# Optimization experiments

Measured on AMD Instinct MI355X. Metric: run time of the kernel, lower is better.

Reference implementation:

```python
import jax, jax.numpy as jnp
import numpy as np

N, L, D = 8192, 50, 64          # batch nodes, history length, embed_dim
NUM_ITEMS, NUM_ATTRS, NUM_FAM = 50000, 100000, 100000


def setup_inputs() -> dict:
    key = jax.random.key(0)
    ks = jax.random.split(key, 12)
    scale = 0.05
    return {
        "nodes": jax.random.randint(ks[0], (N,), 0, NUM_ITEMS),
        "history_va": jax.random.randint(ks[1], (N, L), 0, NUM_ATTRS),
        "history_af": jax.random.randint(ks[2], (N, L), 0, NUM_FAM),
        "v2e_w": jax.random.normal(ks[3], (NUM_ITEMS, D), jnp.float32) * scale,
        "a2e_w": jax.random.normal(ks[4], (NUM_ATTRS, D), jnp.float32) * scale,
        "f2e_w": jax.random.normal(ks[5], (NUM_FAM, D), jnp.float32) * scale,
        "W1": jax.random.normal(ks[6], (3 * D, D), jnp.float32) * scale,
        "b1": jnp.zeros((D,), jnp.float32),
        "W2": jax.random.normal(ks[7], (D, D), jnp.float32) * scale,
        "b2": jnp.zeros((D,), jnp.float32),
        "w3": jax.random.normal(ks[8], (D, 1), jnp.float32) * scale,
        "b3": jnp.zeros((1,), jnp.float32),
    }


def reference(nodes, history_va, history_af, v2e_w, a2e_w, f2e_w,
              W1, b1, W2, b2, w3, b3):
    # Batched form of the per-node loop (va=True branch).
    e_va = a2e_w[history_va]                       # [N, L, D] gathered attr embeds
    e_af = f2e_w[history_af]                       # [N, L, D] gathered famous embeds
    va_rep = v2e_w[nodes]                          # [N, D]    target item embed
    rep = jnp.broadcast_to(va_rep[:, None, :], e_va.shape)
    x = jnp.concatenate([e_va, rep, e_af], axis=-1)  # [N, L, 3D]
    h = jax.nn.relu(x @ W1 + b1)                   # [N, L, D]
    h = jax.nn.relu(h @ W2 + b2)                   # [N, L, D]
    scores = (h @ w3 + b3)[..., 0]                 # [N, L]
    att = jax.nn.softmax(scores, axis=1)           # softmax over history dim
    # e_va.T @ att per node  ==  weighted sum over history
    return jnp.einsum("nld,nl->nd", e_va, att)     # [N, D]
```

## Files before the change

### kernel.cpp

```cpp
#include <hip/hip_runtime.h>
#include <hip/hip_bf16.h>

typedef __bf16    bf16x8 __attribute__((ext_vector_type(8)));
typedef __bf16    bf16x4 __attribute__((ext_vector_type(4)));
typedef _Float16  f16x8  __attribute__((ext_vector_type(8)));
typedef _Float16  f16x4  __attribute__((ext_vector_type(4)));
typedef _Float16  f16x2  __attribute__((ext_vector_type(2)));
typedef float     f32x4  __attribute__((ext_vector_type(4)));

#define HL 50
#define DD 64


__global__ __launch_bounds__(256, 4) void prep_all_kernel(
    const int*   __restrict__ nodes,
    const float* __restrict__ v2e,
    const float* __restrict__ a2e,
    const float* __restrict__ f2e,
    const float* __restrict__ W1,
    const float* __restrict__ b1,
    const float* __restrict__ W2,
    const float* __restrict__ b2,
    const float* __restrict__ w3,
    _Float16* __restrict__ A2, _Float16* __restrict__ F2,
    _Float16* __restrict__ E16, _Float16* __restrict__ ba16,
    _Float16* __restrict__ w2f, float* __restrict__ wsc,
    int nA, int nF, int N, int GA, int GF, int GB)
{
    __shared__ __align__(16) _Float16 wlds[8 * 512];
    __shared__ __align__(16) _Float16 es[64 * 72];
    const int tid  = threadIdx.x;
    const int w    = tid >> 6, lane = tid & 63;
    const int lq   = lane & 15, quad = lane >> 4;
    const int bid  = blockIdx.x;

    if (bid < GA + GF) {
        const bool  isA   = (bid < GA);
        const int   rb    = isA ? bid : bid - GA;
        const int   nrows = isA ? nA : nF;
        const float* src  = isA ? a2e : f2e;
        const float* Wp   = isA ? W1 : (W1 + 128 * DD);
        _Float16*   dst   = isA ? A2 : F2;
        const int   r0w   = rb * 64 + w * 16;
        _Float16*   ws_   = &es[w * 16 * 72];

        float4 v[4];
        int    grv[4];
        #pragma unroll
        for (int i = 0; i < 4; ++i) {
            int t = i * 64 + lane;
            int row = t >> 4, chunk = t & 15;
            int gr = r0w + row; if (gr >= nrows) gr = nrows - 1;
            grv[i] = gr;
            v[i] = *(const float4*)(src + (size_t)gr * DD + chunk * 4);
        }

        #pragma unroll
        for (int h = 0; h < 2; ++h) {
            int combo = w + 4 * h;
            int ct = combo >> 1, t = combo & 1;
            f16x8 pk;
            #pragma unroll
            for (int j = 0; j < 8; ++j)
                pk[j] = (_Float16)Wp[(t * 32 + quad * 8 + j) * DD + ct * 16 + lq];
            *(f16x8*)&wlds[(size_t)combo * 512 + lane * 8] = pk;
        }

        #pragma unroll
        for (int i = 0; i < 4; ++i) {
            int t = i * 64 + lane;
            int row = t >> 4, chunk = t & 15;
            f16x4 pk = {(_Float16)v[i].x, (_Float16)v[i].y,
                        (_Float16)v[i].z, (_Float16)v[i].w};
            *(f16x4*)&ws_[row * 72 + chunk * 4] = pk;
            if (isA) *(f16x4*)(E16 + (size_t)grv[i] * DD + chunk * 4) = pk;
        }

        __syncthreads();

        f16x8 afr[2];
        #pragma unroll
        for (int t = 0; t < 2; ++t)
            afr[t] = *(const f16x8*)&ws_[lq * 72 + t * 32 + quad * 8];
        f32x4 acc[4];
        #pragma unroll
        for (int ct = 0; ct < 4; ++ct) {
            acc[ct] = (f32x4){0.f, 0.f, 0.f, 0.f};
            #pragma unroll
            for (int t = 0; t < 2; ++t) {
                f16x8 bfr = *(const f16x8*)&wlds[(size_t)(ct * 2 + t) * 512 + lane * 8];
                acc[ct] = __builtin_amdgcn_mfma_f32_16x16x32_f16(afr[t], bfr, acc[ct], 0, 0, 0);
            }
        }

        #pragma unroll
        for (int ct = 0; ct < 4; ++ct)
            #pragma unroll
            for (int r = 0; r < 4; ++r)
                ws_[(quad * 4 + r) * 72 + ct * 16 + lq] = (_Float16)acc[ct][r];
        {
            int row = lane >> 2, g = lane & 3;
            int gr  = r0w + row;
            if (gr < nrows) {
                f16x8 v0 = *(const f16x8*)&ws_[row * 72 + g * 16];
                f16x8 v1 = *(const f16x8*)&ws_[row * 72 + g * 16 + 8];
                *(f16x8*)(dst + (size_t)gr * DD + g * 16)     = v0;
                *(f16x8*)(dst + (size_t)gr * DD + g * 16 + 8) = v1;
            }
        }
    } else if (bid < GA + GF + GB) {
        const int col = w * 16 + lq;
        const int n0 = (bid - GA - GF) * 64;
        #pragma unroll
        for (int i = 0; i < 4; ++i) {
            int t = i * 256 + tid;
            int row = t >> 4, q = t & 15;
            int gn = n0 + row; if (gn >= N) gn = N - 1;
            int idx = nodes[gn];
            float4 v = *(const float4*)(v2e + (size_t)idx * DD + q * 4);
            f16x4 pk = {(_Float16)v.x, (_Float16)v.y, (_Float16)v.z, (_Float16)v.w};
            *(f16x4*)&es[row * 72 + q * 4] = pk;
        }
        f16x8 bfr[2];
        #pragma unroll
        for (int t = 0; t < 2; ++t)
            #pragma unroll
            for (int j = 0; j < 8; ++j)
                bfr[t][j] = (_Float16)W1[(64 + t * 32 + quad * 8 + j) * DD + col];
        const float b1c = b1[col];
        __syncthreads();

        f32x4 acc[4];
        #pragma unroll
        for (int mt = 0; mt < 4; ++mt) acc[mt] = (f32x4){0.f, 0.f, 0.f, 0.f};
        #pragma unroll
        for (int t = 0; t < 2; ++t)
            #pragma unroll
            for (int mt = 0; mt < 4; ++mt) {
                f16x8 a = *(const f16x8*)&es[(mt * 16 + lq) * 72 + t * 32 + quad * 8];
                acc[mt] = __builtin_amdgcn_mfma_f32_16x16x32_f16(a, bfr[t], acc[mt], 0, 0, 0);
            }
        #pragma unroll
        for (int mt = 0; mt < 4; ++mt)
            #pragma unroll
            for (int r = 0; r < 4; ++r) {
                int gn = n0 + mt * 16 + quad * 4 + r;
                if (gn < N) ba16[(size_t)gn * DD + col] = (_Float16)(acc[mt][r] + b1c);
            }
    } else {
        const int ln = tid & 63, c0 = tid >> 6;
        #pragma unroll
        for (int h = 0; h < 2; ++h) {
            int combo = c0 + 4 * h;
            int ct = combo >> 1, t = combo & 1;
            _Float16* d = w2f + ((size_t)combo * 64 + ln) * 8;
            #pragma unroll
            for (int j = 0; j < 8; ++j)
                d[j] = (_Float16)W2[(t * 32 + (ln >> 4) * 8 + j) * DD + ct * 16 + (ln & 15)];
        }
        if (tid < 64) { wsc[tid] = w3[tid]; wsc[64 + tid] = b2[tid]; }
    }
}

__global__ __launch_bounds__(256, 4) void va_main_kernel(
    const int*      __restrict__ hva,
    const int*      __restrict__ haf,
    const _Float16* __restrict__ A2,
    const _Float16* __restrict__ F2,
    const _Float16* __restrict__ E16,
    const _Float16* __restrict__ ba16,
    const _Float16* __restrict__ w2f,
    const float*    __restrict__ wsc,
    float*          __restrict__ out, int Ntot)
{
    const int tid  = threadIdx.x;
    const int w    = tid >> 6;
    const int lane = tid & 63;
    const int lq   = lane & 15;
    const int quad = lane >> 4;
    const int node = blockIdx.x * 4 + w;
    if (node >= Ntot) return;

    const int* hb = hva + node * HL;
    const int* fb = haf + node * HL;
    const int lclamp = (lane < HL) ? lane : 0;
    const int iv  = hb[lclamp];
    const int ifv = fb[lclamp];

    f16x8 bag[2];
    #pragma unroll
    for (int t = 0; t < 2; ++t)
        bag[t] = *(const f16x8*)(ba16 + (size_t)node * DD + t * 32 + quad * 8);

    f16x8 a2g[4][2], f2g[4][2];
    #pragma unroll
    for (int mt = 0; mt < 4; ++mt) {
        const int row = mt * 16 + lq;
        const int ia  = __shfl(iv,  row);
        const int ifm = __shfl(ifv, row);
        const bool valid = (row < HL);
        #pragma unroll
        for (int t = 0; t < 2; ++t) {
            if (valid) {
                a2g[mt][t] = *(const f16x8*)(A2 + (size_t)ia  * DD + t * 32 + quad * 8);
                f2g[mt][t] = *(const f16x8*)(F2 + (size_t)ifm * DD + t * 32 + quad * 8);
            }
        }
    }

    f16x2 ev[25];
    #pragma unroll
    for (int i = 0; i < 25; ++i) {
        const int i0 = __builtin_amdgcn_readlane(iv, 2 * i);
        const int i1 = __builtin_amdgcn_readlane(iv, 2 * i + 1);
        ev[i][0] = E16[(size_t)i0 * DD + lane];
        ev[i][1] = E16[(size_t)i1 * DD + lane];
    }

    f16x8 h1f[4][2];
    #pragma unroll
    for (int mt = 0; mt < 4; ++mt) {
        const bool valid = (mt * 16 + lq) < HL;
        #pragma unroll
        for (int t = 0; t < 2; ++t) {
            f16x8 h = a2g[mt][t] + f2g[mt][t] + bag[t];
            #pragma unroll
            for (int j = 0; j < 8; ++j)
                h1f[mt][t][j] = (valid && h[j] > (_Float16)0.f) ? h[j] : (_Float16)0.f;
        }
    }

    float sc[4][4];
    #pragma unroll
    for (int mt = 0; mt < 4; ++mt)
        #pragma unroll
        for (int r = 0; r < 4; ++r) sc[mt][r] = 0.f;

    #pragma unroll
    for (int ct = 0; ct < 4; ++ct) {
        const float b2c = wsc[64 + ct * 16 + lq];
        const float w3c = wsc[ct * 16 + lq];
        f16x8 bfr[2];
        #pragma unroll
        for (int t = 0; t < 2; ++t)
            bfr[t] = *(const f16x8*)(w2f + ((size_t)(ct * 2 + t) * 64 + lane) * 8);
        #pragma unroll
        for (int mt = 0; mt < 4; ++mt) {
            f32x4 acc = {b2c, b2c, b2c, b2c};
            #pragma unroll
            for (int t = 0; t < 2; ++t)
                acc = __builtin_amdgcn_mfma_f32_16x16x32_f16(h1f[mt][t], bfr[t], acc, 0, 0, 0);
            #pragma unroll
            for (int r = 0; r < 4; ++r)
                sc[mt][r] = fmaf(fmaxf(acc[r], 0.f), w3c, sc[mt][r]);
        }
    }

    #pragma unroll
    for (int mt = 0; mt < 4; ++mt)
        #pragma unroll
        for (int r = 0; r < 4; ++r)
            #pragma unroll
            for (int m = 1; m < 16; m <<= 1)
                sc[mt][r] += __shfl_xor(sc[mt][r], m);

    #pragma unroll
    for (int r = 0; r < 4; ++r)
        if (48 + quad * 4 + r >= HL) sc[3][r] = -3.0e38f;

    float mx = sc[0][0];
    #pragma unroll
    for (int mt = 0; mt < 4; ++mt)
        #pragma unroll
        for (int r = 0; r < 4; ++r) mx = fmaxf(mx, sc[mt][r]);
    mx = fmaxf(mx, __shfl_xor(mx, 16));
    mx = fmaxf(mx, __shfl_xor(mx, 32));

    float sm = 0.f;
    #pragma unroll
    for (int mt = 0; mt < 4; ++mt)
        #pragma unroll
        for (int r = 0; r < 4; ++r) {
            sc[mt][r] = __expf(sc[mt][r] - mx);
            sm += sc[mt][r];
        }
    sm += __shfl_xor(sm, 16);
    sm += __shfl_xor(sm, 32);
    const float inv = 1.f / sm;

    float oa[4] = {0.f, 0.f, 0.f, 0.f};
    #pragma unroll
    for (int l = 0; l < HL; ++l) {
        const int   srcl = ((l >> 2) & 3) << 4;
        const float av   = __shfl(sc[l >> 4][l & 3], srcl);
        oa[l & 3] = fmaf(av, (float)ev[l >> 1][l & 1], oa[l & 3]);
    }
    out[(size_t)node * DD + lane] = ((oa[0] + oa[1]) + (oa[2] + oa[3])) * inv;
}

#define FMR  112
#define FMT  7
#define FXSS 136

__global__ __launch_bounds__(256) void fb_prep_kernel(
    const float* __restrict__ W1, const float* __restrict__ W2,
    const float* __restrict__ w3, const float* __restrict__ b1,
    const float* __restrict__ b2,
    __bf16* __restrict__ wf, float* __restrict__ wsc)
{
    const int tid  = threadIdx.x;
    const int quad = tid >> 6;
    const int col  = tid & 63;
    __bf16* dst = wf + tid * 64;
    #pragma unroll
    for (int t = 0; t < 4; ++t)
        #pragma unroll
        for (int j = 0; j < 8; ++j) {
            int keff = t * 32 + quad * 8 + j;
            int krow = (keff < 64) ? keff : keff + 64;
            dst[t * 8 + j] = (__bf16)W1[krow * 64 + col];
        }
    #pragma unroll
    for (int t = 0; t < 2; ++t)
        #pragma unroll
        for (int j = 0; j < 8; ++j) {
            dst[32 + t * 8 + j] = (__bf16)W1[(64 + t * 32 + quad * 8 + j) * 64 + col];
            dst[48 + t * 8 + j] = (__bf16)W2[(t * 32 + quad * 8 + j) * 64 + col];
        }
    if (tid < 64) {
        wsc[tid] = w3[tid]; wsc[64 + tid] = b1[tid]; wsc[128 + tid] = b2[tid];
    }
}

__global__ __launch_bounds__(256, 5) void fb_agg_kernel(
    const int* __restrict__ nodes, const int* __restrict__ hva,
    const int* __restrict__ haf, const float* __restrict__ v2e,
    const float* __restrict__ a2e, const float* __restrict__ f2e,
    const __bf16* __restrict__ wf, const float* __restrict__ wsc,
    float* __restrict__ out)
{
    __shared__ __bf16 xs[FMR * FXSS];
    __shared__ float  pbuf[4 * FMR];
    const int tid = threadIdx.x;
    const int w = tid >> 6, lane = tid & 63, lq = lane & 15, quad = lane >> 4;
    const int col = w * 16 + lq;
    const int n0 = blockIdx.x * 2;
    {
        const int* hb = hva + n0 * HL;
        const int* fb = haf + n0 * HL;
        #pragma unroll
        for (int i = 0; i < 13; ++i) {
            int t = i * 256 + tid;
            if (t < 2 * HL * 2 * 16) {
                int r = t >> 4, q = t & 15;
                bool va = (r < 2 * HL);
                int gr = va ? r : r - 2 * HL;
                int idx = va ? hb[gr] : fb[gr];
                const float* src = (va ? a2e : f2e) + (size_t)idx * DD + q * 4;
                float4 v = *(const float4*)src;
                bf16x4 pk = {(__bf16)v.x, (__bf16)v.y, (__bf16)v.z, (__bf16)v.w};
                *(bf16x4*)&xs[gr * FXSS + (va ? 0 : DD) + q * 4] = pk;
            }
        }
    }
    bf16x8 repf[2];
    #pragma unroll
    for (int t = 0; t < 2; ++t)
        #pragma unroll
        for (int j = 0; j < 8; ++j) repf[t][j] = (__bf16)0.f;
    if (lq < 2) {
        int nd = nodes[n0 + lq];
        const float* rp = v2e + (size_t)nd * DD;
        #pragma unroll
        for (int t = 0; t < 2; ++t) {
            float4 v0 = *(const float4*)(rp + t * 32 + quad * 8);
            float4 v1 = *(const float4*)(rp + t * 32 + quad * 8 + 4);
            repf[t] = (bf16x8){(__bf16)v0.x, (__bf16)v0.y, (__bf16)v0.z, (__bf16)v0.w,
                               (__bf16)v1.x, (__bf16)v1.y, (__bf16)v1.z, (__bf16)v1.w};
        }
    }
    const __bf16* fbp = wf + (size_t)(quad * 64 + col) * 64;
    bf16x8 b1f[4], b1u[2], b2f[2];
    #pragma unroll
    for (int t = 0; t < 4; ++t) b1f[t] = *(const bf16x8*)(fbp + t * 8);
    #pragma unroll
    for (int t = 0; t < 2; ++t) {
        b1u[t] = *(const bf16x8*)(fbp + 32 + t * 8);
        b2f[t] = *(const bf16x8*)(fbp + 48 + t * 8);
    }
    const float w3c = wsc[col];
    const float b1c = wsc[64 + col];
    const float b2c = wsc[128 + col];
    f32x4 rb = {0.f, 0.f, 0.f, 0.f};
    #pragma unroll
    for (int t = 0; t < 2; ++t)
        rb = __builtin_amdgcn_mfma_f32_16x16x32_bf16(repf[t], b1u[t], rb, 0, 0, 0);
    const float bias0 = __shfl(rb[0], lq) + b1c;
    const float bias1 = __shfl(rb[1], lq) + b1c;
    __syncthreads();
    f32x4 acc[FMT];
    #pragma unroll
    for (int mt = 0; mt < FMT; ++mt)
        #pragma unroll
        for (int r = 0; r < 4; ++r) {
            int gr = mt * 16 + quad * 4 + r;
            acc[mt][r] = (gr >= HL) ? bias1 : bias0;
        }
    #pragma unroll
    for (int t = 0; t < 4; ++t)
        #pragma unroll
        for (int mt = 0; mt < FMT; ++mt) {
            bf16x8 a = *(const bf16x8*)&xs[(mt * 16 + lq) * FXSS + t * 32 + quad * 8];
            acc[mt] = __builtin_amdgcn_mfma_f32_16x16x32_bf16(a, b1f[t], acc[mt], 0, 0, 0);
        }
    __syncthreads();
    #pragma unroll
    for (int mt = 0; mt < FMT; ++mt)
        #pragma unroll
        for (int r = 0; r < 4; ++r) {
            int gr = mt * 16 + quad * 4 + r;
            xs[gr * FXSS + DD + col] = (__bf16)fmaxf(acc[mt][r], 0.f);
        }
    __syncthreads();
    f32x4 a2[FMT];
    #pragma unroll
    for (int mt = 0; mt < FMT; ++mt) a2[mt] = (f32x4){b2c, b2c, b2c, b2c};
    #pragma unroll
    for (int t = 0; t < 2; ++t)
        #pragma unroll
        for (int mt = 0; mt < FMT; ++mt) {
            bf16x8 a = *(const bf16x8*)&xs[(mt * 16 + lq) * FXSS + DD + t * 32 + quad * 8];
            a2[mt] = __builtin_amdgcn_mfma_f32_16x16x32_bf16(a, b2f[t], a2[mt], 0, 0, 0);
        }
    #pragma unroll
    for (int mt = 0; mt < FMT; ++mt) {
        float p0 = fmaxf(a2[mt][0], 0.f) * w3c;
        float p1 = fmaxf(a2[mt][1], 0.f) * w3c;
        float p2 = fmaxf(a2[mt][2], 0.f) * w3c;
        float p3 = fmaxf(a2[mt][3], 0.f) * w3c;
        #pragma unroll
        for (int m = 1; m < 16; m <<= 1) {
            p0 += __shfl_xor(p0, m); p1 += __shfl_xor(p1, m);
            p2 += __shfl_xor(p2, m); p3 += __shfl_xor(p3, m);
        }
        if (lq == 0) {
            int rowb = mt * 16 + quad * 4;
            pbuf[w * FMR + rowb + 0] = p0; pbuf[w * FMR + rowb + 1] = p1;
            pbuf[w * FMR + rowb + 2] = p2; pbuf[w * FMR + rowb + 3] = p3;
        }
    }
    __syncthreads();
    const int n = w & 1, lh = w >> 1;
    float att;
    {
        float s = -3.0e38f;
        if (lane < HL) {
            int gr = n * HL + lane;
            s = pbuf[gr] + pbuf[FMR + gr] + pbuf[2 * FMR + gr] + pbuf[3 * FMR + gr];
        }
        float mx = s;
        #pragma unroll
        for (int m = 1; m < 64; m <<= 1) mx = fmaxf(mx, __shfl_xor(mx, m));
        float e = (lane < HL) ? __expf(s - mx) : 0.f;
        float sm = e;
        #pragma unroll
        for (int m = 1; m < 64; m <<= 1) sm += __shfl_xor(sm, m);
        att = e / sm;
    }
    {
        float o = 0.f;
        const int lb = lh * 25;
        #pragma unroll
        for (int i = 0; i < 25; ++i) {
            int l = lb + i;
            float av = __shfl(att, l);
            o = fmaf(av, (float)xs[(n * HL + l) * FXSS + lane], o);
        }
        float* op = (float*)&xs[(100 + w) * FXSS + DD];
        op[lane] = o;
    }
    __syncthreads();
    if (w < 2) {
        const float* p0 = (const float*)&xs[(100 + w) * FXSS + DD];
        const float* p1 = (const float*)&xs[(100 + w + 2) * FXSS + DD];
        out[(size_t)(n0 + w) * DD + lane] = p0[lane] + p1[lane];
    }
}

extern "C" void kernel_launch(void* const* d_in, const int* in_sizes, int n_in,
                              void* d_out, int out_size, void* d_ws, size_t ws_size,
                              hipStream_t stream) {
    const int*   nodes = (const int*)d_in[0];
    const int*   hva   = (const int*)d_in[1];
    const int*   haf   = (const int*)d_in[2];
    const float* v2e   = (const float*)d_in[3];
    const float* a2e   = (const float*)d_in[4];
    const float* f2e   = (const float*)d_in[5];
    const float* W1    = (const float*)d_in[6];
    const float* b1    = (const float*)d_in[7];
    const float* W2    = (const float*)d_in[8];
    const float* b2    = (const float*)d_in[9];
    const float* w3    = (const float*)d_in[10];
    float* out = (float*)d_out;

    const int N  = in_sizes[0];
    const int nA = in_sizes[4] / DD;
    const int nF = in_sizes[5] / DD;

    size_t offA2 = 0;
    size_t offF2 = (offA2 + (size_t)nA * DD * 2 + 255) & ~(size_t)255;
    size_t offE  = (offF2 + (size_t)nF * DD * 2 + 255) & ~(size_t)255;
    size_t offBA = (offE  + (size_t)nA * DD * 2 + 255) & ~(size_t)255;
    size_t offWF = (offBA + (size_t)N * DD * 2 + 255) & ~(size_t)255;
    size_t offSC = offWF + 8 * 64 * 8 * 2;
    size_t need  = offSC + 128 * 4;

    if (ws_size >= need) {
        _Float16* A2  = (_Float16*)((char*)d_ws + offA2);
        _Float16* F2  = (_Float16*)((char*)d_ws + offF2);
        _Float16* E16 = (_Float16*)((char*)d_ws + offE);
        _Float16* ba  = (_Float16*)((char*)d_ws + offBA);
        _Float16* w2f = (_Float16*)((char*)d_ws + offWF);
        float*    wsc = (float*)((char*)d_ws + offSC);

        const int GA = (nA + 63) / 64;
        const int GF = (nF + 63) / 64;
        const int GB = (N + 63) / 64;
        prep_all_kernel<<<GA + GF + GB + 1, 256, 0, stream>>>(
            nodes, v2e, a2e, f2e, W1, b1, W2, b2, w3,
            A2, F2, E16, ba, w2f, wsc, nA, nF, N, GA, GF, GB);
        va_main_kernel<<<(N + 3) / 4, 256, 0, stream>>>(
            hva, haf, A2, F2, E16, ba, w2f, wsc, out, N);
    } else {
        __bf16* wf  = (__bf16*)d_ws;
        float*  wsc = (float*)((char*)d_ws + 256 * 64 * 2);
        fb_prep_kernel<<<1, 256, 0, stream>>>(W1, W2, w3, b1, b2, wf, wsc);
        fb_agg_kernel<<<N / 2, 256, 0, stream>>>(nodes, hva, haf, v2e, a2e, f2e,
                                                 wf, wsc, out);
    }
}
```

Measured before the change: 157.4 us.

## Persistent grid-stride table transform with prefetch; stream E16 loads in main kernel

The prep kernel's A/F table transform now uses a fixed pool of 448 blocks per table. Each block walks tiles in a grid-stride loop and prefetches the next tile's rows into registers while it runs the MFMA on the current one. This amortises the weight-fragment setup and overlaps global loads with compute. The main kernel stops preloading all 50 E16 values into registers and instead loads them inside the weighted-sum loop. Its launch bound is raised to 6 blocks per CU to trade register pressure for occupancy, at the risk of exposing gather latency in that loop.

```diff
diff --git a/kernel.cpp b/kernel.cpp
--- a/kernel.cpp
+++ b/kernel.cpp
@@ -5,7 +5,6 @@
 typedef __bf16    bf16x4 __attribute__((ext_vector_type(4)));
 typedef _Float16  f16x8  __attribute__((ext_vector_type(8)));
 typedef _Float16  f16x4  __attribute__((ext_vector_type(4)));
-typedef _Float16  f16x2  __attribute__((ext_vector_type(2)));
 typedef float     f32x4  __attribute__((ext_vector_type(4)));
 
 #define HL 50
@@ -25,7 +24,7 @@
     _Float16* __restrict__ A2, _Float16* __restrict__ F2,
     _Float16* __restrict__ E16, _Float16* __restrict__ ba16,
     _Float16* __restrict__ w2f, float* __restrict__ wsc,
-    int nA, int nF, int N, int GA, int GF, int GB)
+    int nA, int nF, int N, int GAF, int GB)
 {
     __shared__ __align__(16) _Float16 wlds[8 * 512];
     __shared__ __align__(16) _Float16 es[64 * 72];
@@ -34,26 +33,27 @@
     const int lq   = lane & 15, quad = lane >> 4;
     const int bid  = blockIdx.x;
 
-    if (bid < GA + GF) {
-        const bool  isA   = (bid < GA);
-        const int   rb    = isA ? bid : bid - GA;
+    if (bid < 2 * GAF) {
+        const bool  isA   = (bid < GAF);
+        const int   t0    = isA ? bid : bid - GAF;
         const int   nrows = isA ? nA : nF;
+        const int   NT    = (nrows + 63) >> 6;
         const float* src  = isA ? a2e : f2e;
         const float* Wp   = isA ? W1 : (W1 + 128 * DD);
         _Float16*   dst   = isA ? A2 : F2;
-        const int   r0w   = rb * 64 + w * 16;
         _Float16*   ws_   = &es[w * 16 * 72];
 
-        float4 v[4];
-        int    grv[4];
-        #pragma unroll
-        for (int i = 0; i < 4; ++i) {
-            int t = i * 64 + lane;
-            int row = t >> 4, chunk = t & 15;
-            int gr = r0w + row; if (gr >= nrows) gr = nrows - 1;
-            grv[i] = gr;
-            v[i] = *(const float4*)(src + (size_t)gr * DD + chunk * 4);
-        }
+        auto loadtile = [&](int tb, float4 (&vv)[4], int (&gg)[4]) {
+            const int r0w = tb * 64 + w * 16;
+            #pragma unroll
+            for (int i = 0; i < 4; ++i) {
+                int t = i * 64 + lane;
+                int row = t >> 4, chunk = t & 15;
+                int gr = r0w + row; if (gr >= nrows) gr = nrows - 1;
+                gg[i] = gr;
+                vv[i] = *(const float4*)(src + (size_t)gr * DD + chunk * 4);
+            }
+        };
 
         #pragma unroll
         for (int h = 0; h < 2; ++h) {
@@ -66,51 +66,70 @@
             *(f16x8*)&wlds[(size_t)combo * 512 + lane * 8] = pk;
         }
 
-        #pragma unroll
-        for (int i = 0; i < 4; ++i) {
-            int t = i * 64 + lane;
-            int row = t >> 4, chunk = t & 15;
-            f16x4 pk = {(_Float16)v[i].x, (_Float16)v[i].y,
-                        (_Float16)v[i].z, (_Float16)v[i].w};
-            *(f16x4*)&ws_[row * 72 + chunk * 4] = pk;
-            if (isA) *(f16x4*)(E16 + (size_t)grv[i] * DD + chunk * 4) = pk;
-        }
+        int    tb = t0;
+        float4 v[4];
+        int    grv[4];
+        loadtile(tb, v, grv);
 
         __syncthreads();
 
-        f16x8 afr[2];
-        #pragma unroll
-        for (int t = 0; t < 2; ++t)
-            afr[t] = *(const f16x8*)&ws_[lq * 72 + t * 32 + quad * 8];
-        f32x4 acc[4];
-        #pragma unroll
-        for (int ct = 0; ct < 4; ++ct) {
-            acc[ct] = (f32x4){0.f, 0.f, 0.f, 0.f};
-            #pragma unroll
-            for (int t = 0; t < 2; ++t) {
-                f16x8 bfr = *(const f16x8*)&wlds[(size_t)(ct * 2 + t) * 512 + lane * 8];
-                acc[ct] = __builtin_amdgcn_mfma_f32_16x16x32_f16(afr[t], bfr, acc[ct], 0, 0, 0);
-            }
-        }
-
-        #pragma unroll
-        for (int ct = 0; ct < 4; ++ct)
-            #pragma unroll
-            for (int r = 0; r < 4; ++r)
-                ws_[(quad * 4 + r) * 72 + ct * 16 + lq] = (_Float16)acc[ct][r];
-        {
-            int row = lane >> 2, g = lane & 3;
-            int gr  = r0w + row;
-            if (gr < nrows) {
-                f16x8 v0 = *(const f16x8*)&ws_[row * 72 + g * 16];
-                f16x8 v1 = *(const f16x8*)&ws_[row * 72 + g * 16 + 8];
-                *(f16x8*)(dst + (size_t)gr * DD + g * 16)     = v0;
-                *(f16x8*)(dst + (size_t)gr * DD + g * 16 + 8) = v1;
-            }
-        }
-    } else if (bid < GA + GF + GB) {
+        for (;;) {
+            const int r0w = tb * 64 + w * 16;
+
+            #pragma unroll
+            for (int i = 0; i < 4; ++i) {
+                int t = i * 64 + lane;
+                int row = t >> 4, chunk = t & 15;
+                f16x4 pk = {(_Float16)v[i].x, (_Float16)v[i].y,
+                            (_Float16)v[i].z, (_Float16)v[i].w};
+                *(f16x4*)&ws_[row * 72 + chunk * 4] = pk;
+                if (isA) *(f16x4*)(E16 + (size_t)grv[i] * DD + chunk * 4) = pk;
+            }
+
+            const int tn = tb + GAF;
+            float4 vn[4];
+            int    grn[4];
+            if (tn < NT) loadtile(tn, vn, grn);
+
+            f16x8 afr[2];
+            #pragma unroll
+            for (int t = 0; t < 2; ++t)
+                afr[t] = *(const f16x8*)&ws_[lq * 72 + t * 32 + quad * 8];
+            f32x4 acc[4];
+            #pragma unroll
+            for (int ct = 0; ct < 4; ++ct) {
+                acc[ct] = (f32x4){0.f, 0.f, 0.f, 0.f};
+                #pragma unroll
+                for (int t = 0; t < 2; ++t) {
+                    f16x8 bfr = *(const f16x8*)&wlds[(size_t)(ct * 2 + t) * 512 + lane * 8];
+                    acc[ct] = __builtin_amdgcn_mfma_f32_16x16x32_f16(afr[t], bfr, acc[ct], 0, 0, 0);
+                }
+            }
+
+            #pragma unroll
+            for (int ct = 0; ct < 4; ++ct)
+                #pragma unroll
+                for (int r = 0; r < 4; ++r)
+                    ws_[(quad * 4 + r) * 72 + ct * 16 + lq] = (_Float16)acc[ct][r];
+            {
+                int row = lane >> 2, g = lane & 3;
+                int gr  = r0w + row;
+                if (gr < nrows) {
+                    f16x8 v0 = *(const f16x8*)&ws_[row * 72 + g * 16];
+                    f16x8 v1 = *(const f16x8*)&ws_[row * 72 + g * 16 + 8];
+                    *(f16x8*)(dst + (size_t)gr * DD + g * 16)     = v0;
+                    *(f16x8*)(dst + (size_t)gr * DD + g * 16 + 8) = v1;
+                }
+            }
+
+            if (tn >= NT) break;
+            tb = tn;
+            #pragma unroll
+            for (int i = 0; i < 4; ++i) { v[i] = vn[i]; grv[i] = grn[i]; }
+        }
+    } else if (bid < 2 * GAF + GB) {
         const int col = w * 16 + lq;
-        const int n0 = (bid - GA - GF) * 64;
+        const int n0 = (bid - 2 * GAF) * 64;
         #pragma unroll
         for (int i = 0; i < 4; ++i) {
             int t = i * 256 + tid;
@@ -162,7 +181,7 @@
     }
 }
 
-__global__ __launch_bounds__(256, 4) void va_main_kernel(
+__global__ __launch_bounds__(256, 6) void va_main_kernel(
     const int*      __restrict__ hva,
     const int*      __restrict__ haf,
     const _Float16* __restrict__ A2,
@@ -208,15 +227,6 @@
         }
     }
 
-    f16x2 ev[25];
-    #pragma unroll
-    for (int i = 0; i < 25; ++i) {
-        const int i0 = __builtin_amdgcn_readlane(iv, 2 * i);
-        const int i1 = __builtin_amdgcn_readlane(iv, 2 * i + 1);
-        ev[i][0] = E16[(size_t)i0 * DD + lane];
-        ev[i][1] = E16[(size_t)i1 * DD + lane];
-    }
-
     f16x8 h1f[4][2];
     #pragma unroll
     for (int mt = 0; mt < 4; ++mt) {
@@ -293,7 +303,8 @@
     for (int l = 0; l < HL; ++l) {
         const int   srcl = ((l >> 2) & 3) << 4;
         const float av   = __shfl(sc[l >> 4][l & 3], srcl);
-        oa[l & 3] = fmaf(av, (float)ev[l >> 1][l & 1], oa[l & 3]);
+        const int   idx  = __builtin_amdgcn_readlane(iv, l);
+        oa[l & 3] = fmaf(av, (float)E16[(size_t)idx * DD + lane], oa[l & 3]);
     }
     out[(size_t)node * DD + lane] = ((oa[0] + oa[1]) + (oa[2] + oa[3])) * inv;
 }
@@ -523,12 +534,11 @@
         _Float16* w2f = (_Float16*)((char*)d_ws + offWF);
         float*    wsc = (float*)((char*)d_ws + offSC);
 
-        const int GA = (nA + 63) / 64;
-        const int GF = (nF + 63) / 64;
-        const int GB = (N + 63) / 64;
-        prep_all_kernel<<<GA + GF + GB + 1, 256, 0, stream>>>(
+        const int GAF = 448;
+        const int GB  = (N + 63) / 64;
+        prep_all_kernel<<<2 * GAF + GB + 1, 256, 0, stream>>>(
             nodes, v2e, a2e, f2e, W1, b1, W2, b2, w3,
-            A2, F2, E16, ba, w2f, wsc, nA, nF, N, GA, GF, GB);
+            A2, F2, E16, ba, w2f, wsc, nA, nF, N, GAF, GB);
         va_main_kernel<<<(N + 3) / 4, 256, 0, stream>>>(
             hva, haf, A2, F2, E16, ba, w2f, wsc, out, N);
     } else {
```

Result: slower. 164.4 us (+4.4%).
